# Kernel optimization log

Measured on AMD Instinct MI355X. Metric: run time of the kernel, lower is better.

## Reference

```python
import jax, jax.numpy as jnp
import numpy as np

NH, DH, DHR = 16, 128, 64  # heads, head dim, decoupled rope dim
ROPE_BASE = 10000.0

def _rope(x):
    # x: (B, L, H, Dr) with Dr even; interleaved-pair RoPE (torchtune style)
    B, L, H, Dr = x.shape
    pos = jnp.arange(L, dtype=jnp.float32)
    inv_freq = 1.0 / (ROPE_BASE ** (jnp.arange(0, Dr, 2, dtype=jnp.float32) / Dr))
    ang = pos[:, None] * inv_freq[None, :]          # (L, Dr/2)
    cos = jnp.cos(ang)[None, :, None, :].astype(x.dtype)
    sin = jnp.sin(ang)[None, :, None, :].astype(x.dtype)
    x1, x2 = x[..., 0::2], x[..., 1::2]
    out = jnp.stack([x1 * cos - x2 * sin, x1 * sin + x2 * cos], axis=-1)
    return out.reshape(B, L, H, Dr)

def setup_inputs() -> dict:
    key = jax.random.key(0)
    ks = jax.random.split(key, 9)
    s = 0.02
    return {
        'x':     jax.random.normal(ks[0], (2, 2048, 2048), jnp.float32),
        'W_DKV': jax.random.normal(ks[1], (2048, 682), jnp.float32) * s,
        'W_UK':  jax.random.normal(ks[2], (682, 2048), jnp.float32) * s,
        'W_UV':  jax.random.normal(ks[3], (682, 2048), jnp.float32) * s,
        'W_KR':  jax.random.normal(ks[4], (2048, 64), jnp.float32) * s,
        'W_DQ':  jax.random.normal(ks[5], (2048, 682), jnp.float32) * s,
        'W_UQ':  jax.random.normal(ks[6], (682, 2048), jnp.float32) * s,
        'W_QR':  jax.random.normal(ks[7], (682, 1024), jnp.float32) * s,
        'W_O':   jax.random.normal(ks[8], (2048, 2048), jnp.float32) * s,
    }

def reference(x, W_DKV, W_UK, W_UV, W_KR, W_DQ, W_UQ, W_QR, W_O):
    B, L, D = x.shape
    # --- KV path ---
    c_KV = x @ W_DKV                                   # (B, L, dc)
    k_C = (c_KV @ W_UK).reshape(B, L, NH, DH)          # content keys
    k_R = _rope((x @ W_KR).reshape(B, L, 1, DHR))      # shared rope key head
    k_R = jnp.broadcast_to(k_R, (B, L, NH, DHR))
    k = jnp.concatenate([k_C, k_R], axis=-1)           # (B, L, NH, DH+DHR)
    v = (c_KV @ W_UV).reshape(B, L, NH, DH)
    # --- Q path ---
    c_Q = x @ W_DQ                                     # (B, L, dc')
    q_C = (c_Q @ W_UQ).reshape(B, L, NH, DH)
    q_R = _rope((c_Q @ W_QR).reshape(B, L, NH, DHR))
    q = jnp.concatenate([q_C, q_R], axis=-1)           # (B, L, NH, DH+DHR)
    # --- attention (causal) ---
    scale = 1.0 / jnp.sqrt(jnp.float32(DH + DHR))
    scores = jnp.einsum('blhd,bmhd->bhlm', q, k) * scale
    causal = jnp.tril(jnp.ones((L, L), dtype=bool))
    scores = jnp.where(causal[None, None], scores, jnp.finfo(scores.dtype).min)
    attn = jax.nn.softmax(scores, axis=-1)
    o = jnp.einsum('bhlm,bmhd->blhd', attn, v).reshape(B, L, NH * DH)
    return o @ W_O
```

## Files before the change

kernel.cpp:

```cpp
#include <hip/hip_runtime.h>
#include <stdint.h>

typedef __attribute__((ext_vector_type(8))) __bf16 bf16x8;
typedef __attribute__((ext_vector_type(4))) float f32x4;

#define DEVI static __device__ __forceinline__

DEVI uint16_t f2b(float f) {
  uint32_t u = __float_as_uint(f);
  u += 0x7FFFu + ((u >> 16) & 1u);
  return (uint16_t)(u >> 16);
}
DEVI float b2f(uint16_t b) { return __uint_as_float(((uint32_t)b) << 16); }

DEVI void gl_lds16(const void* g, void* l) {
  __builtin_amdgcn_global_load_lds((const __attribute__((address_space(1))) void*)g,
                                   (__attribute__((address_space(3))) void*)l, 16, 0, 0);
}

DEVI f32x4 mfma16(bf16x8 a, bf16x8 b, f32x4 c) {
  return __builtin_amdgcn_mfma_f32_16x16x32_bf16(a, b, c, 0, 0, 0);
}

#define BARX asm volatile("s_barrier" ::: "memory")
#define WLG0 asm volatile("s_waitcnt lgkmcnt(0)" ::: "memory")
#define WV4 asm volatile("s_waitcnt vmcnt(4)" ::: "memory")
#define PRIO1 __builtin_amdgcn_s_setprio(1)
#define PRIO0 __builtin_amdgcn_s_setprio(0)

__global__ void cast_kernel(const float* __restrict__ X, uint16_t* __restrict__ Y) {
  int id = blockIdx.x * 256 + threadIdx.x;
  float4 v = ((const float4*)X)[id];
  uint16_t o[4] = {f2b(v.x), f2b(v.y), f2b(v.z), f2b(v.w)};
  *(uint64_t*)&Y[(size_t)id * 4] = *(uint64_t*)o;
}

__global__ void wt_kernel(const float* __restrict__ W, uint16_t* __restrict__ Wt,
                          int Kw, int Nw, int Kp, int Np) {
  __shared__ uint16_t T[64][72];
  const int t = threadIdx.x;
  const int n0 = blockIdx.x * 64, k0 = blockIdx.y * 64;
#pragma unroll
  for (int p = 0; p < 2; ++p) {
    int r = p * 32 + (t >> 3);
    int c0 = (t & 7) * 8;
    int gr = k0 + r;
#pragma unroll
    for (int e = 0; e < 8; ++e) {
      int gc = n0 + c0 + e;
      float v = (gr < Kw && gc < Nw) ? W[(size_t)gr * Nw + gc] : 0.f;
      T[c0 + e][r] = f2b(v);
    }
  }
  __syncthreads();
#pragma unroll
  for (int p = 0; p < 2; ++p) {
    int dr = p * 32 + (t >> 3);
    int mc = (t & 7) * 8;
    uint16_t tmp[8];
#pragma unroll
    for (int e = 0; e < 8; ++e) tmp[e] = T[dr][mc + e];
    *(uint64_t*)&Wt[(size_t)(n0 + dr) * Kp + k0 + mc] = ((uint64_t*)tmp)[0];
    *(uint64_t*)&Wt[(size_t)(n0 + dr) * Kp + k0 + mc + 4] = ((uint64_t*)tmp)[1];
  }
}

template <int BM, bool F32OUT>
__global__ __launch_bounds__(512, 2) void gemm8(const uint16_t* __restrict__ A, int lda,
                                                const uint16_t* __restrict__ Bt,
                                                void* __restrict__ Cv, int ldc, int K) {
  constexpr int MF = BM / 32;
  constexpr int MH = MF / 2;
  constexpr int AL = BM / 128;
  constexpr int ABYTES = BM * 128;
  __shared__ char lds[2 * BM * 128 + 2 * 256 * 128];
  char* const LB = lds + 2 * ABYTES;
  const int tid = threadIdx.x;
  const int lane = tid & 63;
  const int lr = lane & 15, lgb = (lane >> 4) * 16;
  const int wid = tid >> 6;
  const int g = wid >> 2;
  const int wc = (wid & 3) * 64;
  const int rA0 = g * (BM / 2) + lr;
  const int rB0 = wc + lr;
  const size_t row0 = (size_t)blockIdx.y * BM, col0 = (size_t)blockIdx.x * 256;
  const char* Agb = (const char*)(A + row0 * lda);
  const char* Btb = (const char*)(Bt + col0 * K);
  const size_t ldab = (size_t)lda * 2;
  const size_t ldbb = (size_t)K * 2;
  const int nk = K >> 6;
  const int ni = nk >> 1;

  f32x4 acc[MF][4] = {};
  bf16x8 aF[MH][2], bF[4][2];

  auto stageA = [&](int kt, int buf, int hf) {
#pragma unroll
    for (int j = 0; j < AL; ++j) {
      int c = j * 512 + tid;
      int cl = c ^ (((c >> 5) & 1) << 1);
      int row = hf * (BM / 2) + (cl >> 3);
      gl_lds16(Agb + (size_t)row * ldab + (size_t)kt * 128 + (cl & 7) * 16,
               lds + buf * ABYTES + hf * (ABYTES / 2) + (j * 512 + (tid & 0x1C0)) * 16);
    }
  };
  auto stageB = [&](int kt, int buf, int hf) {
#pragma unroll
    for (int j = 0; j < 2; ++j) {
      int c = j * 512 + tid;
      int cl = c ^ (((c >> 5) & 1) << 1);
      int row = hf * 128 + (cl >> 3);
      gl_lds16(Btb + (size_t)row * ldbb + (size_t)kt * 128 + (cl & 7) * 16,
               LB + buf * 32768 + hf * 16384 + (j * 512 + (tid & 0x1C0)) * 16);
    }
  };
  auto ldAm = [&](int buf, int mb) {
#pragma unroll
    for (int m = 0; m < MH; ++m) {
      int r = rA0 + (mb + m) * 16;
      int ro = r * 128;
      int sw = ((r >> 2) & 1) << 5;
#pragma unroll
      for (int kk = 0; kk < 2; ++kk)
        aF[m][kk] = *(const bf16x8*)(lds + buf * ABYTES + ((ro + kk * 64 + lgb) ^ sw));
    }
  };
  auto ldBn = [&](int buf, int nb) {
#pragma unroll
    for (int n = 0; n < 2; ++n) {
      int r = rB0 + (nb + n) * 16;
      int ro = r * 128;
      int sw = ((r >> 2) & 1) << 5;
#pragma unroll
      for (int kk = 0; kk < 2; ++kk)
        bF[nb + n][kk] = *(const bf16x8*)(LB + buf * 32768 + ((ro + kk * 64 + lgb) ^ sw));
    }
  };
  auto mmac = [&](int mb, int nb) {
#pragma unroll
    for (int m = 0; m < MH; ++m)
#pragma unroll
      for (int n = 0; n < 2; ++n)
#pragma unroll
        for (int kk = 0; kk < 2; ++kk)
          acc[mb + m][nb + n] = mfma16(aF[m][kk], bF[nb + n][kk], acc[mb + m][nb + n]);
  };

  stageA(0, 0, 0); stageA(0, 0, 1); stageB(0, 0, 0); stageB(0, 0, 1);
  stageB(1, 1, 0); stageB(1, 1, 1);
  WV4; BARX;

  for (int i = 0; i < ni; ++i) {
    const int t1 = 2 * i + 1;
    const int tn = (2 * i + 2 < nk) ? 2 * i + 2 : nk - 1;
    const int tn1 = (2 * i + 3 < nk) ? 2 * i + 3 : nk - 1;
    ldAm(0, 0); ldBn(0, 0); stageA(t1, 1, 0);
    BARX; WLG0; PRIO1; mmac(0, 0); PRIO0; BARX;
    ldBn(0, 2); stageA(t1, 1, 1);
    BARX; WLG0; PRIO1; mmac(0, 2); PRIO0; BARX;
    ldAm(0, MH); stageB(tn, 0, 0);
    BARX; WLG0; PRIO1; mmac(MH, 0); PRIO0; BARX;
    stageB(tn, 0, 1);
    BARX; PRIO1; mmac(MH, 2); PRIO0; WV4; BARX;
    ldAm(1, 0); ldBn(1, 0); stageA(tn, 0, 0);
    BARX; WLG0; PRIO1; mmac(0, 0); PRIO0; BARX;
    ldBn(1, 2); stageA(tn, 0, 1);
    BARX; WLG0; PRIO1; mmac(0, 2); PRIO0; BARX;
    ldAm(1, MH); stageB(tn1, 1, 0);
    BARX; WLG0; PRIO1; mmac(MH, 0); PRIO0; BARX;
    stageB(tn1, 1, 1);
    BARX; PRIO1; mmac(MH, 2); PRIO0; WV4; BARX;
  }
  asm volatile("s_waitcnt vmcnt(0)" ::: "memory");

#pragma unroll
  for (int m = 0; m < MF; ++m)
#pragma unroll
    for (int n = 0; n < 4; ++n)
#pragma unroll
      for (int j = 0; j < 4; ++j) {
        size_t row = row0 + g * (BM / 2) + m * 16 + (lane >> 4) * 4 + j;
        size_t col = col0 + wc + n * 16 + lr;
        if (F32OUT)
          ((float*)Cv)[row * ldc + col] = acc[m][n][j];
        else
          ((uint16_t*)Cv)[row * ldc + col] = f2b(acc[m][n][j]);
      }
}

__global__ void rope_k_kernel(uint16_t* __restrict__ cd) {
  int id = blockIdx.x * 256 + threadIdx.x;
  int row = id >> 5, i = id & 31;
  int pos = row & 2047;
  float invf = exp2f(-13.287712379549449f * (float)i / 32.f);
  float ang = (float)pos * invf;
  float s, c;
  sincosf(ang, &s, &c);
  size_t base = (size_t)row * 1792 + 1536 + 2 * i;
  float x1 = b2f(cd[base]), x2 = b2f(cd[base + 1]);
  cd[base] = f2b(x1 * c - x2 * s);
  cd[base + 1] = f2b(x1 * s + x2 * c);
}

__global__ void rope_q_kernel(uint16_t* __restrict__ cu) {
  int id = blockIdx.x * 256 + threadIdx.x;
  int row = id >> 9;
  int rem = id & 511;
  int h = rem >> 5, i = rem & 31;
  int pos = row & 2047;
  float invf = exp2f(-13.287712379549449f * (float)i / 32.f);
  float ang = (float)pos * invf;
  float s, c;
  sincosf(ang, &s, &c);
  size_t base = (size_t)row * 3072 + 2048 + h * 64 + 2 * i;
  float x1 = b2f(cu[base]), x2 = b2f(cu[base + 1]);
  cu[base] = f2b(x1 * c - x2 * s);
  cu[base + 1] = f2b(x1 * s + x2 * c);
}

__global__ void vtrans_kernel(const uint16_t* __restrict__ v, uint16_t* __restrict__ vt) {
  __shared__ uint16_t T[64][72];
  const int t = threadIdx.x;
  const int mt = blockIdx.x, dt = blockIdx.y, bh = blockIdx.z;
  const int b = bh >> 4, h = bh & 15;
  const int m0 = mt * 64, d0 = dt * 64;
#pragma unroll
  for (int p = 0; p < 2; ++p) {
    int r = p * 32 + (t >> 3), c8 = (t & 7) * 8;
    const uint16_t* s = &v[((size_t)(b * 2048 + m0 + r)) * 4096 + 2048 + h * 128 + d0 + c8];
    uint16_t tmp[8];
    ((uint64_t*)tmp)[0] = ((const uint64_t*)s)[0];
    ((uint64_t*)tmp)[1] = ((const uint64_t*)s)[1];
#pragma unroll
    for (int e = 0; e < 8; ++e) T[c8 + e][r] = tmp[e];
  }
  __syncthreads();
#pragma unroll
  for (int p = 0; p < 2; ++p) {
    int dr = p * 32 + (t >> 3), mc = (t & 7) * 8;
    uint16_t tmp[8];
#pragma unroll
    for (int e = 0; e < 8; ++e) tmp[e] = T[dr][mc + e];
    uint16_t* dstp = &vt[((size_t)(bh * 128 + d0 + dr)) * 2048 + m0 + mc];
    ((uint64_t*)dstp)[0] = ((uint64_t*)tmp)[0];
    ((uint64_t*)dstp)[1] = ((uint64_t*)tmp)[1];
  }
}

__global__ __launch_bounds__(512, 2) void attn_kernel(const uint16_t* __restrict__ cuqr,
                                                      const uint16_t* __restrict__ cukv,
                                                      const uint16_t* __restrict__ cd,
                                                      const uint16_t* __restrict__ vt,
                                                      uint16_t* __restrict__ obuf) {
  __shared__ uint16_t Ks[64 * 192];
  __shared__ uint16_t Vs[128 * 64];
  __shared__ uint16_t Ps[8 * 16 * 64];
  const int tid = threadIdx.x;
  const int wid = tid >> 6, lane = tid & 63;
  const int lr = lane & 15, lg = lane >> 4;
  const int bid = blockIdx.x;
  const int wg = (bid & 7) * 32 + (bid >> 3);
  const int pairi = wg & 7;
  const int bh = wg >> 3;
  const int b = bh >> 4, h = bh & 15;
  const float sc2 = 0.07216878364870323f * 1.4426950408889634f;

  const char* Kcb = (const char*)cukv + (size_t)b * 2048 * 8192 + h * 256;
  const char* Krb = (const char*)cd + (size_t)b * 2048 * 3584 + 3072;
  const char* Vb = (const char*)vt + (size_t)bh * 524288;
  char* KsB = (char*)Ks;
  char* VsB = (char*)Vs;
  char* PwB = (char*)(Ps + wid * 1024);

  const char* kbase[3];
  size_t kstep[3];
  int klds[3];
#pragma unroll
  for (int i = 0; i < 3; ++i) {
    int c = i * 512 + tid;
    int r = c / 24, c16 = c % 24;
    klds[i] = r * 384 + ((c16 * 16) ^ ((r & 7) << 4));
    if (c16 < 16) {
      kbase[i] = Kcb + (size_t)r * 8192 + c16 * 16;
      kstep[i] = (size_t)64 * 8192;
    } else {
      kbase[i] = Krb + (size_t)r * 3584 + (c16 - 16) * 16;
      kstep[i] = (size_t)64 * 3584;
    }
  }
  const char* vbase[2];
  int vlds[2];
#pragma unroll
  for (int i = 0; i < 2; ++i) {
    int c = i * 512 + tid;
    int d = c >> 3, c16 = c & 7;
    vlds[i] = d * 128 + ((c16 * 16) ^ ((d & 7) << 4));
    vbase[i] = Vb + (size_t)d * 4096 + c16 * 16;
  }

  for (int ph = 0; ph < 2; ++ph) {
    const int qt = ph ? (15 - pairi) : pairi;
    const int q0 = qt * 128;
    const int nt = 2 * (qt + 1);
    const int qrow = q0 + wid * 16 + lr;
    bf16x8 qf[6];
    {
      const char* Qcp = (const char*)cuqr + (size_t)(b * 2048 + qrow) * 6144 + h * 256 + lg * 16;
      const char* Qrp =
          (const char*)cuqr + (size_t)(b * 2048 + qrow) * 6144 + 4096 + h * 128 + lg * 16;
#pragma unroll
      for (int kb = 0; kb < 4; ++kb) qf[kb] = *(const bf16x8*)(Qcp + kb * 64);
#pragma unroll
      for (int kb = 0; kb < 2; ++kb) qf[4 + kb] = *(const bf16x8*)(Qrp + kb * 64);
    }
    f32x4 o[8] = {};
    float mrun[4], lrun[4];
#pragma unroll
    for (int j = 0; j < 4; ++j) { mrun[j] = -INFINITY; lrun[j] = 0.f; }

    const char* kp[3];
    const char* vp[2];
    bf16x8 kreg[3], vreg[2];
#pragma unroll
    for (int i = 0; i < 3; ++i) kp[i] = kbase[i];
#pragma unroll
    for (int i = 0; i < 2; ++i) vp[i] = vbase[i];
#pragma unroll
    for (int i = 0; i < 3; ++i) { kreg[i] = *(const bf16x8*)kp[i]; kp[i] += kstep[i]; }
#pragma unroll
    for (int i = 0; i < 2; ++i) { vreg[i] = *(const bf16x8*)vp[i]; vp[i] += 128; }
#pragma unroll
    for (int i = 0; i < 3; ++i) *(bf16x8*)(KsB + klds[i]) = kreg[i];
#pragma unroll
    for (int i = 0; i < 2; ++i) *(bf16x8*)(VsB + vlds[i]) = vreg[i];
    __syncthreads();

    for (int t = 0; t < nt; ++t) {
      const bool more = (t + 1 < nt);
      if (more) {
#pragma unroll
        for (int i = 0; i < 3; ++i) { kreg[i] = *(const bf16x8*)kp[i]; kp[i] += kstep[i]; }
#pragma unroll
        for (int i = 0; i < 2; ++i) { vreg[i] = *(const bf16x8*)vp[i]; vp[i] += 128; }
      }
      if (t * 64 <= q0 + wid * 16 + 15) {
        f32x4 s[4] = {};
        __builtin_amdgcn_s_setprio(1);
#pragma unroll
        for (int n = 0; n < 4; ++n) {
          int r = n * 16 + lr;
          const char* kptr = KsB + r * 384;
          int sw = (r & 7) << 4;
#pragma unroll
          for (int kb = 0; kb < 6; ++kb)
            s[n] = mfma16(qf[kb], *(const bf16x8*)(kptr + ((kb * 64 + lg * 16) ^ sw)), s[n]);
        }
        __builtin_amdgcn_s_setprio(0);
        if (t * 64 + 63 > q0 + wid * 16) {
#pragma unroll
          for (int n = 0; n < 4; ++n)
#pragma unroll
            for (int j = 0; j < 4; ++j)
              if (t * 64 + n * 16 + lr > q0 + wid * 16 + lg * 4 + j) s[n][j] = -INFINITY;
        }
        float pm[4];
#pragma unroll
        for (int j = 0; j < 4; ++j) {
          float v = fmaxf(fmaxf(s[0][j], s[1][j]), fmaxf(s[2][j], s[3][j]));
          v = fmaxf(v, __shfl_xor(v, 1));
          v = fmaxf(v, __shfl_xor(v, 2));
          v = fmaxf(v, __shfl_xor(v, 4));
          v = fmaxf(v, __shfl_xor(v, 8));
          pm[j] = v;
        }
        bool exceed = false;
#pragma unroll
        for (int j = 0; j < 4; ++j) exceed |= (pm[j] > mrun[j] + 76.8f);
        if (__any(exceed)) {
          float alpha[4];
#pragma unroll
          for (int j = 0; j < 4; ++j) {
            float mn = fmaxf(mrun[j], pm[j]);
            alpha[j] = exp2f((mrun[j] - mn) * sc2);
            mrun[j] = mn;
            lrun[j] *= alpha[j];
          }
#pragma unroll
          for (int n2 = 0; n2 < 8; ++n2)
#pragma unroll
            for (int j = 0; j < 4; ++j) o[n2][j] *= alpha[j];
        }
        float rs[4] = {0.f, 0.f, 0.f, 0.f};
#pragma unroll
        for (int n = 0; n < 4; ++n)
#pragma unroll
          for (int j = 0; j < 4; ++j) {
            float p = exp2f((s[n][j] - mrun[j]) * sc2);
            rs[j] += p;
            int row = lg * 4 + j;
            *(uint16_t*)(PwB + row * 128 + ((((n * 16 + lr)) * 2) ^ ((row & 7) << 4))) = f2b(p);
          }
#pragma unroll
        for (int j = 0; j < 4; ++j) {
          float v = rs[j];
          v += __shfl_xor(v, 1);
          v += __shfl_xor(v, 2);
          v += __shfl_xor(v, 4);
          v += __shfl_xor(v, 8);
          lrun[j] += v;
        }
        __builtin_amdgcn_s_setprio(1);
#pragma unroll
        for (int kb2 = 0; kb2 < 2; ++kb2) {
          bf16x8 pa = *(const bf16x8*)(PwB + lr * 128 + ((kb2 * 64 + lg * 16) ^ ((lr & 7) << 4)));
#pragma unroll
          for (int n2 = 0; n2 < 8; ++n2) {
            int vr = n2 * 16 + lr;
            o[n2] = mfma16(
                pa, *(const bf16x8*)(VsB + vr * 128 + ((kb2 * 64 + lg * 16) ^ ((vr & 7) << 4))),
                o[n2]);
          }
        }
        __builtin_amdgcn_s_setprio(0);
      }
      __syncthreads();
      if (more) {
#pragma unroll
        for (int i = 0; i < 3; ++i) *(bf16x8*)(KsB + klds[i]) = kreg[i];
#pragma unroll
        for (int i = 0; i < 2; ++i) *(bf16x8*)(VsB + vlds[i]) = vreg[i];
        __syncthreads();
      }
    }
    float inv[4];
#pragma unroll
    for (int j = 0; j < 4; ++j) inv[j] = 1.f / lrun[j];
#pragma unroll
    for (int n2 = 0; n2 < 8; ++n2)
#pragma unroll
      for (int j = 0; j < 4; ++j) {
        size_t row = (size_t)b * 2048 + q0 + wid * 16 + lg * 4 + j;
        size_t col = (size_t)h * 128 + n2 * 16 + lr;
        obuf[row * 2048 + col] = f2b(o[n2][j] * inv[j]);
      }
  }
}

static constexpr size_t OFF_XB = 0;
static constexpr size_t OFF_WD = 8388608;
static constexpr size_t OFF_WUKV = OFF_WD + 3670016;
static constexpr size_t OFF_WUQR = OFF_WUKV + 3145728;
static constexpr size_t OFF_WO = OFF_WUQR + 2359296;
static constexpr size_t OFF_CD = OFF_WO + 4194304;
static constexpr size_t OFF_CUKV = OFF_CD + 7340032;
static constexpr size_t OFF_CUQR = OFF_CUKV + 16777216;
static constexpr size_t OFF_VT = OFF_CUQR + 12582912;

extern "C" void kernel_launch(void* const* d_in, const int* in_sizes, int n_in,
                              void* d_out, int out_size, void* d_ws, size_t ws_size,
                              hipStream_t stream) {
  (void)in_sizes; (void)n_in; (void)out_size; (void)ws_size;
  const float* x = (const float*)d_in[0];
  const float* Wdkv = (const float*)d_in[1];
  const float* Wuk = (const float*)d_in[2];
  const float* Wuv = (const float*)d_in[3];
  const float* Wkr = (const float*)d_in[4];
  const float* Wdq = (const float*)d_in[5];
  const float* Wuq = (const float*)d_in[6];
  const float* Wqr = (const float*)d_in[7];
  const float* Wo = (const float*)d_in[8];
  uint16_t* ws = (uint16_t*)d_ws;

  uint16_t* xb = ws + OFF_XB;
  uint16_t* obuf = ws + OFF_XB;
  uint16_t* wd = ws + OFF_WD;
  uint16_t* wukv = ws + OFF_WUKV;
  uint16_t* wuqr = ws + OFF_WUQR;
  uint16_t* wo = ws + OFF_WO;
  uint16_t* cd = ws + OFF_CD;
  uint16_t* cukv = ws + OFF_CUKV;
  uint16_t* cuqr = ws + OFF_CUQR;
  uint16_t* vtb = ws + OFF_VT;

  cast_kernel<<<8192, 256, 0, stream>>>(x, xb);
  wt_kernel<<<dim3(12, 32), 256, 0, stream>>>(Wdkv, wd, 2048, 682, 2048, 768);
  wt_kernel<<<dim3(12, 32), 256, 0, stream>>>(Wdq, wd + (size_t)768 * 2048, 2048, 682, 2048, 768);
  wt_kernel<<<dim3(4, 32), 256, 0, stream>>>(Wkr, wd + (size_t)1536 * 2048, 2048, 64, 2048, 256);
  wt_kernel<<<dim3(32, 12), 256, 0, stream>>>(Wuk, wukv, 682, 2048, 768, 2048);
  wt_kernel<<<dim3(32, 12), 256, 0, stream>>>(Wuv, wukv + (size_t)2048 * 768, 682, 2048, 768, 2048);
  wt_kernel<<<dim3(32, 12), 256, 0, stream>>>(Wuq, wuqr, 682, 2048, 768, 2048);
  wt_kernel<<<dim3(16, 12), 256, 0, stream>>>(Wqr, wuqr + (size_t)2048 * 768, 682, 1024, 768, 1024);
  wt_kernel<<<dim3(32, 32), 256, 0, stream>>>(Wo, wo, 2048, 2048, 2048, 2048);
  gemm8<128, false><<<dim3(7, 32), 512, 0, stream>>>(xb, 2048, wd, cd, 1792, 2048);
  gemm8<256, false><<<dim3(16, 16), 512, 0, stream>>>(cd, 1792, wukv, cukv, 4096, 768);
  gemm8<256, false><<<dim3(12, 16), 512, 0, stream>>>(cd + 768, 1792, wuqr, cuqr, 3072, 768);
  rope_k_kernel<<<512, 256, 0, stream>>>(cd);
  rope_q_kernel<<<8192, 256, 0, stream>>>(cuqr);
  vtrans_kernel<<<dim3(32, 2, 32), 256, 0, stream>>>(cukv, vtb);
  attn_kernel<<<256, 512, 0, stream>>>(cuqr, cukv, cd, vtb, obuf);
  gemm8<128, true><<<dim3(8, 32), 512, 0, stream>>>(obuf, 2048, wo, d_out, 2048, 2048);
}
```

Baseline: 306.9 us.

## Simplify GEMM to 4-phase pipeline and split attention pairs across blocks

The GEMM kernel's 8-phase half-tile schedule becomes a simpler 4-phase schedule that loads whole A and B tiles per stage, with per-BM vmcnt waits. This cuts barrier count and instruction overhead per tile, at the cost of coarser overlap between loads and MFMAs. The attention kernel no longer processes a balanced pair of query tiles sequentially in one block. It launches 512 blocks, each handling one query tile, with launch bounds raised to 4 blocks per SM for more parallelism and occupancy. This may cost register pressure and give uneven per-block work.

```diff
diff --git a/kernel.cpp b/kernel.cpp
--- a/kernel.cpp
+++ b/kernel.cpp
@@ -24,7 +24,7 @@
 
 #define BARX asm volatile("s_barrier" ::: "memory")
 #define WLG0 asm volatile("s_waitcnt lgkmcnt(0)" ::: "memory")
-#define WV4 asm volatile("s_waitcnt vmcnt(4)" ::: "memory")
+#define WV0 asm volatile("s_waitcnt vmcnt(0)" ::: "memory")
 #define PRIO1 __builtin_amdgcn_s_setprio(1)
 #define PRIO0 __builtin_amdgcn_s_setprio(0)
 
@@ -66,14 +66,13 @@
 }
 
 template <int BM, bool F32OUT>
-__global__ __launch_bounds__(512, 2) void gemm8(const uint16_t* __restrict__ A, int lda,
+__global__ __launch_bounds__(512, 2) void gemm4(const uint16_t* __restrict__ A, int lda,
                                                 const uint16_t* __restrict__ Bt,
                                                 void* __restrict__ Cv, int ldc, int K) {
   constexpr int MF = BM / 32;
-  constexpr int MH = MF / 2;
-  constexpr int AL = BM / 128;
+  constexpr int AL2 = BM / 64;
   constexpr int ABYTES = BM * 128;
-  __shared__ char lds[2 * BM * 128 + 2 * 256 * 128];
+  __shared__ char lds[2 * ABYTES + 2 * 32768];
   char* const LB = lds + 2 * ABYTES;
   const int tid = threadIdx.x;
   const int lane = tid & 63;
@@ -92,32 +91,30 @@
   const int ni = nk >> 1;
 
   f32x4 acc[MF][4] = {};
-  bf16x8 aF[MH][2], bF[4][2];
-
-  auto stageA = [&](int kt, int buf, int hf) {
-#pragma unroll
-    for (int j = 0; j < AL; ++j) {
+  bf16x8 aF[MF][2], bF[4][2];
+
+  auto stageA = [&](int kt, int buf) {
+#pragma unroll
+    for (int j = 0; j < AL2; ++j) {
       int c = j * 512 + tid;
       int cl = c ^ (((c >> 5) & 1) << 1);
-      int row = hf * (BM / 2) + (cl >> 3);
-      gl_lds16(Agb + (size_t)row * ldab + (size_t)kt * 128 + (cl & 7) * 16,
-               lds + buf * ABYTES + hf * (ABYTES / 2) + (j * 512 + (tid & 0x1C0)) * 16);
+      gl_lds16(Agb + (size_t)(cl >> 3) * ldab + (size_t)kt * 128 + (cl & 7) * 16,
+               lds + buf * ABYTES + (j * 512 + (tid & 0x1C0)) * 16);
     }
   };
-  auto stageB = [&](int kt, int buf, int hf) {
-#pragma unroll
-    for (int j = 0; j < 2; ++j) {
+  auto stageB = [&](int kt, int buf) {
+#pragma unroll
+    for (int j = 0; j < 4; ++j) {
       int c = j * 512 + tid;
       int cl = c ^ (((c >> 5) & 1) << 1);
-      int row = hf * 128 + (cl >> 3);
-      gl_lds16(Btb + (size_t)row * ldbb + (size_t)kt * 128 + (cl & 7) * 16,
-               LB + buf * 32768 + hf * 16384 + (j * 512 + (tid & 0x1C0)) * 16);
+      gl_lds16(Btb + (size_t)(cl >> 3) * ldbb + (size_t)kt * 128 + (cl & 7) * 16,
+               LB + buf * 32768 + (j * 512 + (tid & 0x1C0)) * 16);
     }
   };
-  auto ldAm = [&](int buf, int mb) {
-#pragma unroll
-    for (int m = 0; m < MH; ++m) {
-      int r = rA0 + (mb + m) * 16;
+  auto ldA = [&](int buf) {
+#pragma unroll
+    for (int m = 0; m < MF; ++m) {
+      int r = rA0 + m * 16;
       int ro = r * 128;
       int sw = ((r >> 2) & 1) << 5;
 #pragma unroll
@@ -125,7 +122,7 @@
         aF[m][kk] = *(const bf16x8*)(lds + buf * ABYTES + ((ro + kk * 64 + lgb) ^ sw));
     }
   };
-  auto ldBn = [&](int buf, int nb) {
+  auto ldB = [&](int buf, int nb) {
 #pragma unroll
     for (int n = 0; n < 2; ++n) {
       int r = rB0 + (nb + n) * 16;
@@ -136,42 +133,38 @@
         bF[nb + n][kk] = *(const bf16x8*)(LB + buf * 32768 + ((ro + kk * 64 + lgb) ^ sw));
     }
   };
-  auto mmac = [&](int mb, int nb) {
-#pragma unroll
-    for (int m = 0; m < MH; ++m)
+  auto mmac = [&](int nb) {
+#pragma unroll
+    for (int m = 0; m < MF; ++m)
 #pragma unroll
       for (int n = 0; n < 2; ++n)
 #pragma unroll
         for (int kk = 0; kk < 2; ++kk)
-          acc[mb + m][nb + n] = mfma16(aF[m][kk], bF[nb + n][kk], acc[mb + m][nb + n]);
+          acc[m][nb + n] = mfma16(aF[m][kk], bF[nb + n][kk], acc[m][nb + n]);
   };
 
-  stageA(0, 0, 0); stageA(0, 0, 1); stageB(0, 0, 0); stageB(0, 0, 1);
-  stageB(1, 1, 0); stageB(1, 1, 1);
-  WV4; BARX;
+  stageA(0, 0);
+  stageB(0, 0);
+  WV0;
+  BARX;
 
   for (int i = 0; i < ni; ++i) {
     const int t1 = 2 * i + 1;
-    const int tn = (2 * i + 2 < nk) ? 2 * i + 2 : nk - 1;
-    const int tn1 = (2 * i + 3 < nk) ? 2 * i + 3 : nk - 1;
-    ldAm(0, 0); ldBn(0, 0); stageA(t1, 1, 0);
-    BARX; WLG0; PRIO1; mmac(0, 0); PRIO0; BARX;
-    ldBn(0, 2); stageA(t1, 1, 1);
-    BARX; WLG0; PRIO1; mmac(0, 2); PRIO0; BARX;
-    ldAm(0, MH); stageB(tn, 0, 0);
-    BARX; WLG0; PRIO1; mmac(MH, 0); PRIO0; BARX;
-    stageB(tn, 0, 1);
-    BARX; PRIO1; mmac(MH, 2); PRIO0; WV4; BARX;
-    ldAm(1, 0); ldBn(1, 0); stageA(tn, 0, 0);
-    BARX; WLG0; PRIO1; mmac(0, 0); PRIO0; BARX;
-    ldBn(1, 2); stageA(tn, 0, 1);
-    BARX; WLG0; PRIO1; mmac(0, 2); PRIO0; BARX;
-    ldAm(1, MH); stageB(tn1, 1, 0);
-    BARX; WLG0; PRIO1; mmac(MH, 0); PRIO0; BARX;
-    stageB(tn1, 1, 1);
-    BARX; PRIO1; mmac(MH, 2); PRIO0; WV4; BARX;
-  }
-  asm volatile("s_waitcnt vmcnt(0)" ::: "memory");
+    const int t2 = (2 * i + 2 < nk) ? 2 * i + 2 : nk - 1;
+    ldA(0); ldB(0, 0); stageA(t1, 1); stageB(t1, 1);
+    BARX; WLG0; PRIO1; mmac(0); PRIO0; BARX;
+    ldB(0, 2); stageA(t2, 0);
+    BARX; WLG0; PRIO1; mmac(2); PRIO0;
+    if constexpr (BM == 256)
+      asm volatile("s_waitcnt vmcnt(4)" ::: "memory");
+    else
+      asm volatile("s_waitcnt vmcnt(2)" ::: "memory");
+    BARX;
+    ldA(1); ldB(1, 0); stageB(t2, 0);
+    BARX; WLG0; PRIO1; mmac(0); PRIO0; BARX;
+    ldB(1, 2);
+    BARX; WLG0; PRIO1; mmac(2); PRIO0; WV0; BARX;
+  }
 
 #pragma unroll
   for (int m = 0; m < MF; ++m)
@@ -247,7 +240,7 @@
   }
 }
 
-__global__ __launch_bounds__(512, 2) void attn_kernel(const uint16_t* __restrict__ cuqr,
+__global__ __launch_bounds__(512, 4) void attn_kernel(const uint16_t* __restrict__ cuqr,
                                                       const uint16_t* __restrict__ cukv,
                                                       const uint16_t* __restrict__ cd,
                                                       const uint16_t* __restrict__ vt,
@@ -259,9 +252,11 @@
   const int wid = tid >> 6, lane = tid & 63;
   const int lr = lane & 15, lg = lane >> 4;
   const int bid = blockIdx.x;
-  const int wg = (bid & 7) * 32 + (bid >> 3);
-  const int pairi = wg & 7;
-  const int bh = wg >> 3;
+  const int cpair = bid >> 8, r = bid & 255;
+  const int rp = (r & 7) * 32 + (r >> 3);
+  const int bh = rp >> 3;
+  const int qtl = rp & 7;
+  const int qt = cpair ? (15 - qtl) : qtl;
   const int b = bh >> 4, h = bh & 15;
   const float sc2 = 0.07216878364870323f * 1.4426950408889634f;
 
@@ -272,178 +267,169 @@
   char* VsB = (char*)Vs;
   char* PwB = (char*)(Ps + wid * 1024);
 
-  const char* kbase[3];
+  const char* kp[3];
   size_t kstep[3];
   int klds[3];
 #pragma unroll
   for (int i = 0; i < 3; ++i) {
     int c = i * 512 + tid;
-    int r = c / 24, c16 = c % 24;
-    klds[i] = r * 384 + ((c16 * 16) ^ ((r & 7) << 4));
+    int rr = c / 24, c16 = c % 24;
+    klds[i] = rr * 384 + ((c16 * 16) ^ ((rr & 7) << 4));
     if (c16 < 16) {
-      kbase[i] = Kcb + (size_t)r * 8192 + c16 * 16;
+      kp[i] = Kcb + (size_t)rr * 8192 + c16 * 16;
       kstep[i] = (size_t)64 * 8192;
     } else {
-      kbase[i] = Krb + (size_t)r * 3584 + (c16 - 16) * 16;
+      kp[i] = Krb + (size_t)rr * 3584 + (c16 - 16) * 16;
       kstep[i] = (size_t)64 * 3584;
     }
   }
-  const char* vbase[2];
+  const char* vp[2];
   int vlds[2];
 #pragma unroll
   for (int i = 0; i < 2; ++i) {
     int c = i * 512 + tid;
     int d = c >> 3, c16 = c & 7;
     vlds[i] = d * 128 + ((c16 * 16) ^ ((d & 7) << 4));
-    vbase[i] = Vb + (size_t)d * 4096 + c16 * 16;
-  }
-
-  for (int ph = 0; ph < 2; ++ph) {
-    const int qt = ph ? (15 - pairi) : pairi;
-    const int q0 = qt * 128;
-    const int nt = 2 * (qt + 1);
-    const int qrow = q0 + wid * 16 + lr;
-    bf16x8 qf[6];
-    {
-      const char* Qcp = (const char*)cuqr + (size_t)(b * 2048 + qrow) * 6144 + h * 256 + lg * 16;
-      const char* Qrp =
-          (const char*)cuqr + (size_t)(b * 2048 + qrow) * 6144 + 4096 + h * 128 + lg * 16;
-#pragma unroll
-      for (int kb = 0; kb < 4; ++kb) qf[kb] = *(const bf16x8*)(Qcp + kb * 64);
-#pragma unroll
-      for (int kb = 0; kb < 2; ++kb) qf[4 + kb] = *(const bf16x8*)(Qrp + kb * 64);
-    }
-    f32x4 o[8] = {};
-    float mrun[4], lrun[4];
-#pragma unroll
-    for (int j = 0; j < 4; ++j) { mrun[j] = -INFINITY; lrun[j] = 0.f; }
-
-    const char* kp[3];
-    const char* vp[2];
-    bf16x8 kreg[3], vreg[2];
-#pragma unroll
-    for (int i = 0; i < 3; ++i) kp[i] = kbase[i];
-#pragma unroll
-    for (int i = 0; i < 2; ++i) vp[i] = vbase[i];
-#pragma unroll
-    for (int i = 0; i < 3; ++i) { kreg[i] = *(const bf16x8*)kp[i]; kp[i] += kstep[i]; }
-#pragma unroll
-    for (int i = 0; i < 2; ++i) { vreg[i] = *(const bf16x8*)vp[i]; vp[i] += 128; }
-#pragma unroll
-    for (int i = 0; i < 3; ++i) *(bf16x8*)(KsB + klds[i]) = kreg[i];
-#pragma unroll
-    for (int i = 0; i < 2; ++i) *(bf16x8*)(VsB + vlds[i]) = vreg[i];
+    vp[i] = Vb + (size_t)d * 4096 + c16 * 16;
+  }
+
+  const int q0 = qt * 128;
+  const int nt = 2 * (qt + 1);
+  const int qrow = q0 + wid * 16 + lr;
+  bf16x8 qf[6];
+  {
+    const char* Qcp = (const char*)cuqr + (size_t)(b * 2048 + qrow) * 6144 + h * 256 + lg * 16;
+    const char* Qrp =
+        (const char*)cuqr + (size_t)(b * 2048 + qrow) * 6144 + 4096 + h * 128 + lg * 16;
+#pragma unroll
+    for (int kb = 0; kb < 4; ++kb) qf[kb] = *(const bf16x8*)(Qcp + kb * 64);
+#pragma unroll
+    for (int kb = 0; kb < 2; ++kb) qf[4 + kb] = *(const bf16x8*)(Qrp + kb * 64);
+  }
+  f32x4 o[8] = {};
+  float mrun[4], lrun[4];
+#pragma unroll
+  for (int j = 0; j < 4; ++j) { mrun[j] = -INFINITY; lrun[j] = 0.f; }
+
+  bf16x8 kreg[3], vreg[2];
+#pragma unroll
+  for (int i = 0; i < 3; ++i) { kreg[i] = *(const bf16x8*)kp[i]; kp[i] += kstep[i]; }
+#pragma unroll
+  for (int i = 0; i < 2; ++i) { vreg[i] = *(const bf16x8*)vp[i]; vp[i] += 128; }
+#pragma unroll
+  for (int i = 0; i < 3; ++i) *(bf16x8*)(KsB + klds[i]) = kreg[i];
+#pragma unroll
+  for (int i = 0; i < 2; ++i) *(bf16x8*)(VsB + vlds[i]) = vreg[i];
+  __syncthreads();
+
+  for (int t = 0; t < nt; ++t) {
+    const bool more = (t + 1 < nt);
+    if (more) {
+#pragma unroll
+      for (int i = 0; i < 3; ++i) { kreg[i] = *(const bf16x8*)kp[i]; kp[i] += kstep[i]; }
+#pragma unroll
+      for (int i = 0; i < 2; ++i) { vreg[i] = *(const bf16x8*)vp[i]; vp[i] += 128; }
+    }
+    if (t * 64 <= q0 + wid * 16 + 15) {
+      f32x4 s[4] = {};
+      __builtin_amdgcn_s_setprio(1);
+#pragma unroll
+      for (int n = 0; n < 4; ++n) {
+        int rr = n * 16 + lr;
+        const char* kptr = KsB + rr * 384;
+        int sw = (rr & 7) << 4;
+#pragma unroll
+        for (int kb = 0; kb < 6; ++kb)
+          s[n] = mfma16(qf[kb], *(const bf16x8*)(kptr + ((kb * 64 + lg * 16) ^ sw)), s[n]);
+      }
+      __builtin_amdgcn_s_setprio(0);
+      if (t * 64 + 63 > q0 + wid * 16) {
+#pragma unroll
+        for (int n = 0; n < 4; ++n)
+#pragma unroll
+          for (int j = 0; j < 4; ++j)
+            if (t * 64 + n * 16 + lr > q0 + wid * 16 + lg * 4 + j) s[n][j] = -INFINITY;
+      }
+      float pm[4];
+#pragma unroll
+      for (int j = 0; j < 4; ++j) {
+        float v = fmaxf(fmaxf(s[0][j], s[1][j]), fmaxf(s[2][j], s[3][j]));
+        v = fmaxf(v, __shfl_xor(v, 1));
+        v = fmaxf(v, __shfl_xor(v, 2));
+        v = fmaxf(v, __shfl_xor(v, 4));
+        v = fmaxf(v, __shfl_xor(v, 8));
+        pm[j] = v;
+      }
+      bool exceed = false;
+#pragma unroll
+      for (int j = 0; j < 4; ++j) exceed |= (pm[j] > mrun[j] + 76.8f);
+      if (__any(exceed)) {
+        float alpha[4];
+#pragma unroll
+        for (int j = 0; j < 4; ++j) {
+          float mn = fmaxf(mrun[j], pm[j]);
+          alpha[j] = exp2f((mrun[j] - mn) * sc2);
+          mrun[j] = mn;
+          lrun[j] *= alpha[j];
+        }
+#pragma unroll
+        for (int n2 = 0; n2 < 8; ++n2)
+#pragma unroll
+          for (int j = 0; j < 4; ++j) o[n2][j] *= alpha[j];
+      }
+      float rs[4] = {0.f, 0.f, 0.f, 0.f};
+#pragma unroll
+      for (int n = 0; n < 4; ++n)
+#pragma unroll
+        for (int j = 0; j < 4; ++j) {
+          float p = exp2f((s[n][j] - mrun[j]) * sc2);
+          rs[j] += p;
+          int row = lg * 4 + j;
+          *(uint16_t*)(PwB + row * 128 + ((((n * 16 + lr)) * 2) ^ ((row & 7) << 4))) = f2b(p);
+        }
+#pragma unroll
+      for (int j = 0; j < 4; ++j) {
+        float v = rs[j];
+        v += __shfl_xor(v, 1);
+        v += __shfl_xor(v, 2);
+        v += __shfl_xor(v, 4);
+        v += __shfl_xor(v, 8);
+        lrun[j] += v;
+      }
+      __builtin_amdgcn_s_setprio(1);
+#pragma unroll
+      for (int kb2 = 0; kb2 < 2; ++kb2) {
+        bf16x8 pa = *(const bf16x8*)(PwB + lr * 128 + ((kb2 * 64 + lg * 16) ^ ((lr & 7) << 4)));
+#pragma unroll
+        for (int n2 = 0; n2 < 8; ++n2) {
+          int vr = n2 * 16 + lr;
+          o[n2] = mfma16(
+              pa, *(const bf16x8*)(VsB + vr * 128 + ((kb2 * 64 + lg * 16) ^ ((vr & 7) << 4))),
+              o[n2]);
+        }
+      }
+      __builtin_amdgcn_s_setprio(0);
+    }
     __syncthreads();
-
-    for (int t = 0; t < nt; ++t) {
-      const bool more = (t + 1 < nt);
-      if (more) {
-#pragma unroll
-        for (int i = 0; i < 3; ++i) { kreg[i] = *(const bf16x8*)kp[i]; kp[i] += kstep[i]; }
-#pragma unroll
-        for (int i = 0; i < 2; ++i) { vreg[i] = *(const bf16x8*)vp[i]; vp[i] += 128; }
-      }
-      if (t * 64 <= q0 + wid * 16 + 15) {
-        f32x4 s[4] = {};
-        __builtin_amdgcn_s_setprio(1);
-#pragma unroll
-        for (int n = 0; n < 4; ++n) {
-          int r = n * 16 + lr;
-          const char* kptr = KsB + r * 384;
-          int sw = (r & 7) << 4;
-#pragma unroll
-          for (int kb = 0; kb < 6; ++kb)
-            s[n] = mfma16(qf[kb], *(const bf16x8*)(kptr + ((kb * 64 + lg * 16) ^ sw)), s[n]);
-        }
-        __builtin_amdgcn_s_setprio(0);
-        if (t * 64 + 63 > q0 + wid * 16) {
-#pragma unroll
-          for (int n = 0; n < 4; ++n)
-#pragma unroll
-            for (int j = 0; j < 4; ++j)
-              if (t * 64 + n * 16 + lr > q0 + wid * 16 + lg * 4 + j) s[n][j] = -INFINITY;
-        }
-        float pm[4];
-#pragma unroll
-        for (int j = 0; j < 4; ++j) {
-          float v = fmaxf(fmaxf(s[0][j], s[1][j]), fmaxf(s[2][j], s[3][j]));
-          v = fmaxf(v, __shfl_xor(v, 1));
-          v = fmaxf(v, __shfl_xor(v, 2));
-          v = fmaxf(v, __shfl_xor(v, 4));
-          v = fmaxf(v, __shfl_xor(v, 8));
-          pm[j] = v;
-        }
-        bool exceed = false;
-#pragma unroll
-        for (int j = 0; j < 4; ++j) exceed |= (pm[j] > mrun[j] + 76.8f);
-        if (__any(exceed)) {
-          float alpha[4];
-#pragma unroll
-          for (int j = 0; j < 4; ++j) {
-            float mn = fmaxf(mrun[j], pm[j]);
-            alpha[j] = exp2f((mrun[j] - mn) * sc2);
-            mrun[j] = mn;
-            lrun[j] *= alpha[j];
-          }
-#pragma unroll
-          for (int n2 = 0; n2 < 8; ++n2)
-#pragma unroll
-            for (int j = 0; j < 4; ++j) o[n2][j] *= alpha[j];
-        }
-        float rs[4] = {0.f, 0.f, 0.f, 0.f};
-#pragma unroll
-        for (int n = 0; n < 4; ++n)
-#pragma unroll
-          for (int j = 0; j < 4; ++j) {
-            float p = exp2f((s[n][j] - mrun[j]) * sc2);
-            rs[j] += p;
-            int row = lg * 4 + j;
-            *(uint16_t*)(PwB + row * 128 + ((((n * 16 + lr)) * 2) ^ ((row & 7) << 4))) = f2b(p);
-          }
-#pragma unroll
-        for (int j = 0; j < 4; ++j) {
-          float v = rs[j];
-          v += __shfl_xor(v, 1);
-          v += __shfl_xor(v, 2);
-          v += __shfl_xor(v, 4);
-          v += __shfl_xor(v, 8);
-          lrun[j] += v;
-        }
-        __builtin_amdgcn_s_setprio(1);
-#pragma unroll
-        for (int kb2 = 0; kb2 < 2; ++kb2) {
-          bf16x8 pa = *(const bf16x8*)(PwB + lr * 128 + ((kb2 * 64 + lg * 16) ^ ((lr & 7) << 4)));
-#pragma unroll
-          for (int n2 = 0; n2 < 8; ++n2) {
-            int vr = n2 * 16 + lr;
-            o[n2] = mfma16(
-                pa, *(const bf16x8*)(VsB + vr * 128 + ((kb2 * 64 + lg * 16) ^ ((vr & 7) << 4))),
-                o[n2]);
-          }
-        }
-        __builtin_amdgcn_s_setprio(0);
-      }
+    if (more) {
+#pragma unroll
+      for (int i = 0; i < 3; ++i) *(bf16x8*)(KsB + klds[i]) = kreg[i];
+#pragma unroll
+      for (int i = 0; i < 2; ++i) *(bf16x8*)(VsB + vlds[i]) = vreg[i];
       __syncthreads();
-      if (more) {
-#pragma unroll
-        for (int i = 0; i < 3; ++i) *(bf16x8*)(KsB + klds[i]) = kreg[i];
-#pragma unroll
-        for (int i = 0; i < 2; ++i) *(bf16x8*)(VsB + vlds[i]) = vreg[i];
-        __syncthreads();
-      }
-    }
-    float inv[4];
-#pragma unroll
-    for (int j = 0; j < 4; ++j) inv[j] = 1.f / lrun[j];
-#pragma unroll
-    for (int n2 = 0; n2 < 8; ++n2)
-#pragma unroll
-      for (int j = 0; j < 4; ++j) {
-        size_t row = (size_t)b * 2048 + q0 + wid * 16 + lg * 4 + j;
-        size_t col = (size_t)h * 128 + n2 * 16 + lr;
-        obuf[row * 2048 + col] = f2b(o[n2][j] * inv[j]);
-      }
-  }
+    }
+  }
+  float inv[4];
+#pragma unroll
+  for (int j = 0; j < 4; ++j) inv[j] = 1.f / lrun[j];
+#pragma unroll
+  for (int n2 = 0; n2 < 8; ++n2)
+#pragma unroll
+    for (int j = 0; j < 4; ++j) {
+      size_t row = (size_t)b * 2048 + q0 + wid * 16 + lg * 4 + j;
+      size_t col = (size_t)h * 128 + n2 * 16 + lr;
+      obuf[row * 2048 + col] = f2b(o[n2][j] * inv[j]);
+    }
 }
 
 static constexpr size_t OFF_XB = 0;
@@ -491,12 +477,12 @@
   wt_kernel<<<dim3(32, 12), 256, 0, stream>>>(Wuq, wuqr, 682, 2048, 768, 2048);
   wt_kernel<<<dim3(16, 12), 256, 0, stream>>>(Wqr, wuqr + (size_t)2048 * 768, 682, 1024, 768, 1024);
   wt_kernel<<<dim3(32, 32), 256, 0, stream>>>(Wo, wo, 2048, 2048, 2048, 2048);
-  gemm8<128, false><<<dim3(7, 32), 512, 0, stream>>>(xb, 2048, wd, cd, 1792, 2048);
-  gemm8<256, false><<<dim3(16, 16), 512, 0, stream>>>(cd, 1792, wukv, cukv, 4096, 768);
-  gemm8<256, false><<<dim3(12, 16), 512, 0, stream>>>(cd + 768, 1792, wuqr, cuqr, 3072, 768);
+  gemm4<128, false><<<dim3(7, 32), 512, 0, stream>>>(xb, 2048, wd, cd, 1792, 2048);
+  gemm4<256, false><<<dim3(16, 16), 512, 0, stream>>>(cd, 1792, wukv, cukv, 4096, 768);
+  gemm4<256, false><<<dim3(12, 16), 512, 0, stream>>>(cd + 768, 1792, wuqr, cuqr, 3072, 768);
   rope_k_kernel<<<512, 256, 0, stream>>>(cd);
   rope_q_kernel<<<8192, 256, 0, stream>>>(cuqr);
   vtrans_kernel<<<dim3(32, 2, 32), 256, 0, stream>>>(cukv, vtb);
-  attn_kernel<<<256, 512, 0, stream>>>(cuqr, cukv, cd, vtb, obuf);
-  gemm8<128, true><<<dim3(8, 32), 512, 0, stream>>>(obuf, 2048, wo, d_out, 2048, 2048);
-}
+  attn_kernel<<<512, 512, 0, stream>>>(cuqr, cukv, cd, vtb, obuf);
+  gemm4<128, true><<<dim3(8, 32), 512, 0, stream>>>(obuf, 2048, wo, d_out, 2048, 2048);
+}
```

Result: slower. 566.5 us (+84.6%).
